# Performance work log

Measured on AMD Instinct MI355X. Metric: run time of the kernel, lower is better.

Reference implementation:

```python
import jax, jax.numpy as jnp
import numpy as np

Q_LEN = 2048
K_LEN = 2048
BATCH = 2
EMBED = 1024
HEADS = 16
HEAD_DIM = EMBED // HEADS
PE_ROWS = 2 * K_LEN


def _shift(p):
    # Transformer-XL pad/flatten shift: p is [B, H, Q, S] with S = 2*K-1 -> [B, H, Q, K]
    B, H, Q, S = p.shape
    pp = jnp.pad(p, ((0, 0), (0, 0), (0, 1), (0, 1)))          # [B,H,Q+1,S+1]
    flat = pp.reshape(B, H, (Q + 1) * (S + 1))
    flat = jax.lax.slice_in_dim(flat, S // 2, S // 2 + Q * S, axis=-1)
    return flat.reshape(B, H, Q, S)[..., : (S + 1) // 2]


def setup_inputs() -> dict:
    key = jax.random.key(0)
    ks = jax.random.split(key, 11)
    ws = 0.02  # weight scale
    inp = {
        "query": jax.random.normal(ks[0], (Q_LEN, BATCH, EMBED), jnp.float32),
        "key": jax.random.normal(ks[1], (K_LEN, BATCH, EMBED), jnp.float32),
        "value": jax.random.normal(ks[2], (K_LEN, BATCH, EMBED), jnp.float32),
        "pe": jax.random.normal(ks[3], (PE_ROWS, EMBED), jnp.float32),
        "w_q": jax.random.normal(ks[4], (EMBED, EMBED), jnp.float32) * ws,
        "w_k": jax.random.normal(ks[5], (EMBED, EMBED), jnp.float32) * ws,
        "w_v": jax.random.normal(ks[6], (EMBED, EMBED), jnp.float32) * ws,
        "w_k_pos": jax.random.normal(ks[7], (EMBED, EMBED), jnp.float32) * ws,
        "out_proj": jax.random.normal(ks[8], (EMBED, EMBED), jnp.float32) * ws,
        "content_bias": jax.random.normal(ks[9], (HEADS, HEAD_DIM), jnp.float32) * ws,
        "pos_bias": jax.random.normal(ks[10], (HEADS, HEAD_DIM), jnp.float32) * ws,
        "attn_mask": jnp.triu(jnp.ones((Q_LEN, K_LEN), dtype=bool), k=1),  # causal
    }
    return inp


def reference(query, key, value, pe, w_q, w_k, w_v, w_k_pos, out_proj,
              content_bias, pos_bias, attn_mask):
    Qlen, B, E = query.shape
    Klen = key.shape[0]
    H, D = content_bias.shape
    scaling = D ** -0.5

    # projections (torch Linear: x @ W^T); layout -> [B, H, L, D]
    q = (query @ w_q.T).reshape(Qlen, B, H, D).transpose(1, 2, 0, 3)
    k = (key @ w_k.T).reshape(Klen, B, H, D).transpose(1, 2, 0, 3)
    v = (value @ w_v.T).reshape(Klen, B, H, D).transpose(1, 2, 0, 3)

    # relative position keys: pe slice of size 2K-1 starting at pe.size(0)//2 - K + 1
    lower = pe.shape[0] // 2 - Klen + 1
    pe_slice = jax.lax.dynamic_slice_in_dim(pe, lower, 2 * Klen - 1, axis=0)
    k_pos = (pe_slice @ w_k_pos.T).reshape(2 * Klen - 1, H, D).transpose(1, 0, 2)  # [H, 2K-1, D]

    content = jnp.einsum('bhqd,bhkd->bhqk', q + content_bias[None, :, None, :], k)
    pos = jnp.einsum('bhqd,hsd->bhqs', q + pos_bias[None, :, None, :], k_pos)
    pos = _shift(pos)  # [B, H, Q, K]

    attn = (content + pos) * scaling
    attn = jnp.where(attn_mask[None, None], -jnp.inf, attn)
    w = jax.nn.softmax(attn, axis=-1)

    out = jnp.einsum('bhqk,bhkd->bhqd', w, v)
    out = out.transpose(2, 0, 1, 3).reshape(Qlen, B, E)
    return out @ out_proj.T
```

## Files before the change

### kernel.cpp

```cpp
#include <hip/hip_runtime.h>
#include <hip/hip_bf16.h>

typedef __hip_bfloat16 bf16;
typedef __attribute__((ext_vector_type(8))) short short8;
typedef __attribute__((ext_vector_type(8))) unsigned short u16x8;
typedef __attribute__((ext_vector_type(4))) float f32x4;

#define QL   2048
#define KLEN 2048
#define BATCH 2
#define EMB  1024
#define NH   16
#define HD   64
#define SPE  4095

__device__ int detect_f32(const void* __restrict__ p) {
    const unsigned short* u = (const unsigned short*)p;
    int bad = 0;
    for (int i = 0; i < 256; i++) {
        int e = (u[i] >> 7) & 0xFF;
        if (e >= 0x8A) bad++;
    }
    return bad >= 8;
}

__device__ __forceinline__ ushort4 cvt4(const void* src, long u4i, int f32) {
    ushort4 o;
    if (f32) {
        float4 v = ((const float4*)src)[u4i];
        bf16 a = (bf16)v.x, b = (bf16)v.y, c = (bf16)v.z, e = (bf16)v.w;
        o.x = *(unsigned short*)&a; o.y = *(unsigned short*)&b;
        o.z = *(unsigned short*)&c; o.w = *(unsigned short*)&e;
    } else {
        o = ((const ushort4*)src)[u4i];
    }
    return o;
}

__global__ __launch_bounds__(256) void conv_w(
    const void* w0, const void* w1, const void* w2, const void* w3, const void* w4,
    const void* cb, const void* pb, bf16* __restrict__ dst)
{
    const int t = threadIdx.x;
    const int bid = blockIdx.x;
    __shared__ int f32s;
    if (bid < 1280) {
        const int seg = bid >> 8, inner = bid & 255;
        const void* src = seg == 0 ? w0 : seg == 1 ? w1 : seg == 2 ? w2 : seg == 3 ? w3 : w4;
        bf16* d = dst + (size_t)seg * 1048576;
        if (t == 0) f32s = detect_f32(src);
        __syncthreads();
        const int f32 = f32s;
#pragma unroll
        for (int i = 0; i < 4; i++) {
            long u4i = (long)inner * 1024 + i * 256 + t;
            ((ushort4*)d)[u4i] = cvt4(src, u4i, f32);
        }
    } else {
        if (t == 0) f32s = detect_f32(cb);
        __syncthreads();
        const int f32 = f32s;
        ((ushort4*)(dst + 5242880))[t]        = cvt4(cb, t, f32);
        ((ushort4*)(dst + 5242880 + 1024))[t] = cvt4(pb, t, f32);
    }
}

__global__ __launch_bounds__(256) void conv_act(
    const void* q, const void* k, const void* v, const void* pe,
    bf16* __restrict__ dq, bf16* __restrict__ dk,
    bf16* __restrict__ dv, bf16* __restrict__ dp)
{
    const int t = threadIdx.x;
    const int seg = blockIdx.x >> 10, inner = blockIdx.x & 1023;
    const void* src = seg == 0 ? q : seg == 1 ? k : seg == 2 ? v : pe;
    bf16* d = seg == 0 ? dq : seg == 1 ? dk : seg == 2 ? dv : dp;
    const long srcOff4 = (seg == 3) ? 256 : 0;
    const long zero4   = (seg == 3) ? 1048320 : (1L << 40);
    __shared__ int f32s;
    if (t == 0) f32s = detect_f32(src);
    __syncthreads();
    const int f32 = f32s;
#pragma unroll
    for (int i = 0; i < 4; i++) {
        long u4i = (long)inner * 1024 + i * 256 + t;
        ushort4 o;
        if (u4i >= zero4) { o.x = o.y = o.z = o.w = 0; }
        else o = cvt4(src, srcOff4 + u4i, f32);
        ((ushort4*)d)[u4i] = o;
    }
}

__device__ __forceinline__ void llds16(const bf16* g, bf16* l) {
    __builtin_amdgcn_global_load_lds(
        (const __attribute__((address_space(1))) void*)g,
        (__attribute__((address_space(3))) void*)l,
        16, 0, 0);
}

__global__ __launch_bounds__(256) void gemm_big(
    const bf16* __restrict__ A0, const bf16* __restrict__ A1,
    const bf16* __restrict__ A2, const bf16* __restrict__ A3,
    const bf16* __restrict__ wslab,
    bf16* __restrict__ qc, bf16* __restrict__ qp,
    bf16* __restrict__ kw, bf16* __restrict__ vw,
    bf16* __restrict__ kpos, float* __restrict__ outf, int mode_base)
{
    const int mode = mode_base + blockIdx.z;
    const bf16* A = mode == 0 ? A0 : mode == 1 ? A1 : mode == 2 ? A2 : A3;
    const bf16* W = wslab + (size_t)mode * 1048576;

    __shared__ __align__(16) bf16 Asd[128 * 64];
    __shared__ __align__(16) bf16 Wsd[128 * 64];

    const int t = threadIdx.x;
    const int w = t >> 6, lane = t & 63, lm = lane & 15, quad = lane >> 4;
    const int m0 = blockIdx.x * 128, n0 = blockIdx.y * 128;
    const int wr = (w >> 1) * 64, wc = (w & 1) * 64;

    f32x4 acc[4][4] = {};

    for (int k0 = 0; k0 < 1024; k0 += 64) {
#pragma unroll
        for (int i = 0; i < 4; i++) {
            int c = i * 256 + t, r = c >> 3, ch = c & 7, gc = ch ^ (r & 7);
            llds16(A + (size_t)(m0 + r) * 1024 + k0 + gc * 8, Asd + (c & ~63) * 8);
        }
#pragma unroll
        for (int i = 0; i < 4; i++) {
            int c = i * 256 + t, r = c >> 3, ch = c & 7, gc = ch ^ (r & 7);
            llds16(W + (size_t)(n0 + r) * 1024 + k0 + gc * 8, Wsd + (c & ~63) * 8);
        }
        __syncthreads();

        short8 af[4][2], wf[4][2];
#pragma unroll
        for (int x = 0; x < 4; x++) {
            int ra = wr + x * 16 + lm;
            af[x][0] = *(const short8*)&Asd[ra * 64 + ((quad)     ^ (ra & 7)) * 8];
            af[x][1] = *(const short8*)&Asd[ra * 64 + ((4 + quad) ^ (ra & 7)) * 8];
            int rb = wc + x * 16 + lm;
            wf[x][0] = *(const short8*)&Wsd[rb * 64 + ((quad)     ^ (rb & 7)) * 8];
            wf[x][1] = *(const short8*)&Wsd[rb * 64 + ((4 + quad) ^ (rb & 7)) * 8];
        }
#pragma unroll
        for (int kk = 0; kk < 2; kk++)
#pragma unroll
            for (int mt = 0; mt < 4; mt++)
#pragma unroll
                for (int nt = 0; nt < 4; nt++)
                    acc[mt][nt] = __builtin_amdgcn_mfma_f32_16x16x32_bf16(
                        af[mt][kk], wf[nt][kk], acc[mt][nt], 0, 0, 0);
        __syncthreads();
    }

    const bf16* cbb = wslab + 5242880;
    const bf16* pbb = wslab + 5242880 + 1024;

#pragma unroll
    for (int mt = 0; mt < 4; mt++) {
#pragma unroll
        for (int nt = 0; nt < 4; nt++) {
#pragma unroll
            for (int r4 = 0; r4 < 4; r4++) {
                int row = m0 + wr + mt * 16 + quad * 4 + r4;
                int col = n0 + wc + nt * 16 + lm;
                float v = acc[mt][nt][r4];
                if (mode == 0) {
                    int l = row >> 1, b = row & 1;
                    int h = col >> 6, d = col & 63;
                    size_t idx = ((size_t)(b * NH + h) * QL + l) * HD + d;
                    qc[idx] = (bf16)(v + __bfloat162float(cbb[col]));
                    qp[idx] = (bf16)(v + __bfloat162float(pbb[col]));
                } else if (mode == 1) {
                    int l = row >> 1, b = row & 1;
                    int h = col >> 6, d = col & 63;
                    kw[((size_t)(b * NH + h) * KLEN + l) * HD + d] = (bf16)v;
                } else if (mode == 2) {
                    int l = row >> 1, b = row & 1;
                    int h = col >> 6, d = col & 63;
                    vw[((size_t)(b * NH + h) * KLEN + l) * HD + d] = (bf16)v;
                } else if (mode == 3) {
                    if (row < SPE) {
                        int h = col >> 6, d = col & 63;
                        kpos[((size_t)h * SPE + row) * HD + d] = (bf16)v;
                    }
                } else {
                    outf[(size_t)row * 1024 + col] = v;
                }
            }
        }
    }
}

#define NEG_INF (-1.0e30f)

__global__ __launch_bounds__(256) void attn_mfma(
    const bf16* __restrict__ qc_g, const bf16* __restrict__ qp_g,
    const bf16* __restrict__ k_g,  const bf16* __restrict__ v_g,
    const bf16* __restrict__ kpos_g, bf16* __restrict__ ao)
{
    const int lin = blockIdx.x + (blockIdx.y << 6) + (blockIdx.z << 10);
    const int xcd = lin & 7, s = lin >> 3;
    const int g   = (xcd << 2) | (s >> 6);
    const int bx  = 63 - (s & 63);
    const int h   = g & 15;
    const int b   = g >> 4;
    const int q0  = bx * 32;

    const bf16* qc_bh  = qc_g + ((size_t)(b * NH + h) * QL) * HD;
    const bf16* qp_bh  = qp_g + ((size_t)(b * NH + h) * QL) * HD;
    const bf16* k_bh   = k_g  + ((size_t)(b * NH + h) * KLEN) * HD;
    const bf16* v_bh   = v_g  + ((size_t)(b * NH + h) * KLEN) * HD;
    const bf16* kpos_h = kpos_g + (size_t)h * SPE * HD;

    __shared__ __align__(16) bf16 K_s [64 * 64];
    __shared__ __align__(16) bf16 Kp_s[96 * 64];
    __shared__ __align__(16) bf16 Vt_s[64 * 64];
    __shared__ __align__(16) bf16 Pb_s[32 * 64];
    __shared__ float Sc_s[32][69];
    __shared__ float Pt_s[32][99];
    __shared__ float arow_s[32];

    const int t = threadIdx.x;
    const int w = t >> 6, lane = t & 63, lm = lane & 15, quad = lane >> 4;

    const int sr = t >> 3;
    const int sc = (t & 7) * 8;
    const int vrr = t >> 3, vch = t & 7;
    const int vslot = ((vrr >> 2) ^ vch);

    const int mtc = w & 1;
    const int ntc = (w >> 1) * 2;
    const int mtp = w >> 1;
    const int ntp = (w & 1) * 3;

    float m_run = NEG_INF, l_part = 0.0f;
    f32x4 accO[2] = {{0,0,0,0},{0,0,0,0}};
    u16x8 vv0, vv1;

    const int nkt = (bx >> 1) + 1;

    short8 aQc0, aQc1, aQp0, aQp1;
    {
        const bf16* qr = qc_bh + (size_t)(q0 + mtc * 16 + lm) * HD;
        aQc0 = *(const short8*)(qr + quad * 8);
        aQc1 = *(const short8*)(qr + (4 + quad) * 8);
        const bf16* pr = qp_bh + (size_t)(q0 + mtp * 16 + lm) * HD;
        aQp0 = *(const short8*)(pr + quad * 8);
        aQp1 = *(const short8*)(pr + (4 + quad) * 8);
    }

#pragma unroll
    for (int i = 0; i < 2; i++) {
        int c = i * 256 + t, r = c >> 3, ch = c & 7, gc = ch ^ (r & 7);
        llds16(k_bh + (size_t)r * HD + gc * 8, K_s + (c & ~63) * 8);
    }
    {
        const int s0 = 2016 - q0;
#pragma unroll
        for (int i = 0; i < 3; i++) {
            int c = i * 256 + t, r = c >> 3, ch = c & 7, gc = ch ^ (r & 7);
            llds16(kpos_h + (size_t)(s0 + r) * HD + gc * 8, Kp_s + (c & ~63) * 8);
        }
    }
    vv0 = *(const u16x8*)&v_bh[(size_t)(2 * vrr)     * HD + vch * 8];
    vv1 = *(const u16x8*)&v_bh[(size_t)(2 * vrr + 1) * HD + vch * 8];

    for (int kt = 0; kt < nkt; kt++) {
        const int k0 = kt * 64;

        __syncthreads();

        {
            const int off = (2 * vrr) & 7;
#pragma unroll
            for (int j = 0; j < 8; j++) {
                unsigned int pair = (unsigned int)vv0[j] | ((unsigned int)vv1[j] << 16);
                *(unsigned int*)&Vt_s[(vch * 8 + j) * 64 + vslot * 8 + off] = pair;
            }
        }

        {
#pragma unroll
            for (int n = 0; n < 2; n++) {
                int rowB = (ntc + n) * 16 + lm;
                short8 b0 = *(const short8*)&K_s[rowB * 64 + ((quad)     ^ (rowB & 7)) * 8];
                short8 b1 = *(const short8*)&K_s[rowB * 64 + ((4 + quad) ^ (rowB & 7)) * 8];
                f32x4 acc = {0, 0, 0, 0};
                acc = __builtin_amdgcn_mfma_f32_16x16x32_bf16(aQc0, b0, acc, 0, 0, 0);
                acc = __builtin_amdgcn_mfma_f32_16x16x32_bf16(aQc1, b1, acc, 0, 0, 0);
#pragma unroll
                for (int r = 0; r < 4; r++)
                    Sc_s[mtc * 16 + quad * 4 + r][(ntc + n) * 16 + lm] = acc[r];
            }
        }
        {
#pragma unroll
            for (int n = 0; n < 3; n++) {
                int rowB = (ntp + n) * 16 + lm;
                short8 b0 = *(const short8*)&Kp_s[rowB * 64 + ((quad)     ^ (rowB & 7)) * 8];
                short8 b1 = *(const short8*)&Kp_s[rowB * 64 + ((4 + quad) ^ (rowB & 7)) * 8];
                f32x4 acc = {0, 0, 0, 0};
                acc = __builtin_amdgcn_mfma_f32_16x16x32_bf16(aQp0, b0, acc, 0, 0, 0);
                acc = __builtin_amdgcn_mfma_f32_16x16x32_bf16(aQp1, b1, acc, 0, 0, 0);
#pragma unroll
                for (int r = 0; r < 4; r++)
                    Pt_s[mtp * 16 + quad * 4 + r][(ntp + n) * 16 + lm] = acc[r];
            }
        }

        __syncthreads();

        if (kt + 1 < nkt) {
            const int k0n = k0 + 64;
            const int s0n = k0n - q0 + 2016;
#pragma unroll
            for (int i = 0; i < 2; i++) {
                int c = i * 256 + t, r = c >> 3, ch = c & 7, gc = ch ^ (r & 7);
                llds16(k_bh + (size_t)(k0n + r) * HD + gc * 8, K_s + (c & ~63) * 8);
            }
#pragma unroll
            for (int i = 0; i < 3; i++) {
                int c = i * 256 + t, r = c >> 3, ch = c & 7, gc = ch ^ (r & 7);
                llds16(kpos_h + (size_t)(s0n + r) * HD + gc * 8, Kp_s + (c & ~63) * 8);
            }
            vv0 = *(const u16x8*)&v_bh[(size_t)(k0n + 2 * vrr)     * HD + vch * 8];
            vv1 = *(const u16x8*)&v_bh[(size_t)(k0n + 2 * vrr + 1) * HD + vch * 8];
        }

        {
            float p[8];
            float pmax = NEG_INF;
#pragma unroll
            for (int j = 0; j < 8; j++) {
                int col = sc + j;
                float s = (Sc_s[sr][col] + Pt_s[sr][col - sr + 31]) * 0.125f;
                if (k0 + col > q0 + sr) s = NEG_INF;
                p[j] = s;
                pmax = fmaxf(pmax, s);
            }
            float alpha = 1.0f;
            if (!__all(pmax <= m_run + 8.0f)) {
                float mx = pmax;
                mx = fmaxf(mx, __shfl_xor(mx, 1, 8));
                mx = fmaxf(mx, __shfl_xor(mx, 2, 8));
                mx = fmaxf(mx, __shfl_xor(mx, 4, 8));
                float mnew = fmaxf(m_run, mx);
                alpha = __expf(m_run - mnew);
                m_run = mnew;
            }
            float ls = 0.0f;
#pragma unroll
            for (int j = 0; j < 8; j++) { p[j] = __expf(p[j] - m_run); ls += p[j]; }
            l_part = l_part * alpha + ls;
            if ((t & 7) == 0) arow_s[sr] = alpha;
            short8 pv;
#pragma unroll
            for (int j = 0; j < 8; j++) { bf16 x = (bf16)p[j]; pv[j] = *(short*)&x; }
            *(short8*)&Pb_s[sr * 64 + ((t & 7) ^ (sr & 7)) * 8] = pv;
        }

        asm volatile("s_waitcnt lgkmcnt(0)" ::: "memory");
        __builtin_amdgcn_s_barrier();
        __builtin_amdgcn_sched_barrier(0);

        {
            float al[4];
#pragma unroll
            for (int r = 0; r < 4; r++) al[r] = arow_s[mtc * 16 + quad * 4 + r];
            int rowA = mtc * 16 + lm;
            short8 a0 = *(const short8*)&Pb_s[rowA * 64 + ((quad)     ^ (rowA & 7)) * 8];
            short8 a1 = *(const short8*)&Pb_s[rowA * 64 + ((4 + quad) ^ (rowA & 7)) * 8];
#pragma unroll
            for (int n = 0; n < 2; n++) {
                int d = (ntc + n) * 16 + lm;
                int dc = d >> 3;
                short8 b0 = *(const short8*)&Vt_s[d * 64 + ((quad)     ^ dc) * 8];
                short8 b1 = *(const short8*)&Vt_s[d * 64 + ((4 + quad) ^ dc) * 8];
#pragma unroll
                for (int r = 0; r < 4; r++) accO[n][r] *= al[r];
                accO[n] = __builtin_amdgcn_mfma_f32_16x16x32_bf16(a0, b0, accO[n], 0, 0, 0);
                accO[n] = __builtin_amdgcn_mfma_f32_16x16x32_bf16(a1, b1, accO[n], 0, 0, 0);
            }
        }
    }

    l_part += __shfl_xor(l_part, 1, 8);
    l_part += __shfl_xor(l_part, 2, 8);
    l_part += __shfl_xor(l_part, 4, 8);

    __syncthreads();
    if ((t & 7) == 0) arow_s[sr] = l_part;
    __syncthreads();

    float linv[4];
#pragma unroll
    for (int r = 0; r < 4; r++) linv[r] = 1.0f / arow_s[mtc * 16 + quad * 4 + r];
#pragma unroll
    for (int n = 0; n < 2; n++) {
#pragma unroll
        for (int r = 0; r < 4; r++) {
            int row = mtc * 16 + quad * 4 + r;
            ao[(((size_t)(q0 + row) * BATCH + b) * EMB) + h * HD + (ntc + n) * 16 + lm] =
                (bf16)(accO[n][r] * linv[r]);
        }
    }
}

extern "C" void kernel_launch(void* const* d_in, const int* in_sizes, int n_in,
                              void* d_out, int out_size, void* d_ws, size_t ws_size,
                              hipStream_t stream)
{
    const void* query = d_in[0];
    const void* key   = d_in[1];
    const void* value = d_in[2];
    const void* pe    = d_in[3];
    const void* w_q   = d_in[4];
    const void* w_k   = d_in[5];
    const void* w_v   = d_in[6];
    const void* w_kp  = d_in[7];
    const void* w_out = d_in[8];
    const void* cb    = d_in[9];
    const void* pb    = d_in[10];
    float* out = (float*)d_out;

    const size_t SLAB = 4194304;
    bf16* qc   = (bf16*)d_ws;
    bf16* qp   = qc + SLAB;
    bf16* kw   = qp + SLAB;
    bf16* vw   = kw + SLAB;
    bf16* kpos = vw + SLAB;
    bf16* ao   = kpos + SLAB;
    bf16* stg  = ao + SLAB;
    bf16* wqb  = stg + SLAB;

    bf16* stgQ = (bf16*)d_out;
    bf16* stgV = stgQ + SLAB;

    dim3 blk(256);

    conv_w<<<dim3(1281), blk, 0, stream>>>(w_q, w_k, w_v, w_kp, w_out, cb, pb, wqb);
    conv_act<<<dim3(4096), blk, 0, stream>>>(query, key, value, pe, stgQ, stg, stgV, ao);

    gemm_big<<<dim3(32, 8, 4), blk, 0, stream>>>(
        stgQ, stg, stgV, ao, wqb, qc, qp, kw, vw, kpos, nullptr, 0);

    attn_mfma<<<dim3(64, NH, BATCH), blk, 0, stream>>>(qc, qp, kw, vw, kpos, ao);

    gemm_big<<<dim3(32, 8, 1), blk, 0, stream>>>(
        stgQ, stg, stgV, ao, wqb, qc, qp, kw, vw, kpos, out, 4);
}
```

Before: 367.9 us.

## Fuse conversion kernels, triple-buffer GEMM, remap blocks, use exp2 softmax

Merges the weight and activation conversion kernels into one launch. Rewrites the projection GEMM as a triple-buffered K=32 pipeline with asynchronous LDS loads, and remaps workgroups across XCDs. In attention, the scale is folded into log2 units so the softmax can use exp2, and query blocks are interleaved for load balance. The V-transpose LDS swizzle and padding are also changed to reduce bank conflicts. In exchange, the GEMM loop has more iterations with more barriers, and the softmax threshold change shifts how often rescaling happens.

```diff
diff --git a/kernel.cpp b/kernel.cpp
--- a/kernel.cpp
+++ b/kernel.cpp
@@ -37,9 +37,12 @@
     return o;
 }
 
-__global__ __launch_bounds__(256) void conv_w(
+__global__ __launch_bounds__(256) void conv_all(
     const void* w0, const void* w1, const void* w2, const void* w3, const void* w4,
-    const void* cb, const void* pb, bf16* __restrict__ dst)
+    const void* cb, const void* pb, bf16* __restrict__ wdst,
+    const void* q, const void* k, const void* v, const void* pe,
+    bf16* __restrict__ dq, bf16* __restrict__ dk,
+    bf16* __restrict__ dv, bf16* __restrict__ dp)
 {
     const int t = threadIdx.x;
     const int bid = blockIdx.x;
@@ -47,7 +50,7 @@
     if (bid < 1280) {
         const int seg = bid >> 8, inner = bid & 255;
         const void* src = seg == 0 ? w0 : seg == 1 ? w1 : seg == 2 ? w2 : seg == 3 ? w3 : w4;
-        bf16* d = dst + (size_t)seg * 1048576;
+        bf16* d = wdst + (size_t)seg * 1048576;
         if (t == 0) f32s = detect_f32(src);
         __syncthreads();
         const int f32 = f32s;
@@ -56,37 +59,30 @@
             long u4i = (long)inner * 1024 + i * 256 + t;
             ((ushort4*)d)[u4i] = cvt4(src, u4i, f32);
         }
-    } else {
+    } else if (bid == 1280) {
         if (t == 0) f32s = detect_f32(cb);
         __syncthreads();
         const int f32 = f32s;
-        ((ushort4*)(dst + 5242880))[t]        = cvt4(cb, t, f32);
-        ((ushort4*)(dst + 5242880 + 1024))[t] = cvt4(pb, t, f32);
-    }
-}
-
-__global__ __launch_bounds__(256) void conv_act(
-    const void* q, const void* k, const void* v, const void* pe,
-    bf16* __restrict__ dq, bf16* __restrict__ dk,
-    bf16* __restrict__ dv, bf16* __restrict__ dp)
-{
-    const int t = threadIdx.x;
-    const int seg = blockIdx.x >> 10, inner = blockIdx.x & 1023;
-    const void* src = seg == 0 ? q : seg == 1 ? k : seg == 2 ? v : pe;
-    bf16* d = seg == 0 ? dq : seg == 1 ? dk : seg == 2 ? dv : dp;
-    const long srcOff4 = (seg == 3) ? 256 : 0;
-    const long zero4   = (seg == 3) ? 1048320 : (1L << 40);
-    __shared__ int f32s;
-    if (t == 0) f32s = detect_f32(src);
-    __syncthreads();
-    const int f32 = f32s;
-#pragma unroll
-    for (int i = 0; i < 4; i++) {
-        long u4i = (long)inner * 1024 + i * 256 + t;
-        ushort4 o;
-        if (u4i >= zero4) { o.x = o.y = o.z = o.w = 0; }
-        else o = cvt4(src, srcOff4 + u4i, f32);
-        ((ushort4*)d)[u4i] = o;
+        ((ushort4*)(wdst + 5242880))[t]        = cvt4(cb, t, f32);
+        ((ushort4*)(wdst + 5242880 + 1024))[t] = cvt4(pb, t, f32);
+    } else {
+        const int abid = bid - 1281;
+        const int seg = abid >> 10, inner = abid & 1023;
+        const void* src = seg == 0 ? q : seg == 1 ? k : seg == 2 ? v : pe;
+        bf16* d = seg == 0 ? dq : seg == 1 ? dk : seg == 2 ? dv : dp;
+        const long srcOff4 = (seg == 3) ? 256 : 0;
+        const long zero4   = (seg == 3) ? 1048320 : (1L << 40);
+        if (t == 0) f32s = detect_f32(src);
+        __syncthreads();
+        const int f32 = f32s;
+#pragma unroll
+        for (int i = 0; i < 4; i++) {
+            long u4i = (long)inner * 1024 + i * 256 + t;
+            ushort4 o;
+            if (u4i >= zero4) { o.x = o.y = o.z = o.w = 0; }
+            else o = cvt4(src, srcOff4 + u4i, f32);
+            ((ushort4*)d)[u4i] = o;
+        }
     }
 }
 
@@ -105,52 +101,65 @@
     bf16* __restrict__ kw, bf16* __restrict__ vw,
     bf16* __restrict__ kpos, float* __restrict__ outf, int mode_base)
 {
-    const int mode = mode_base + blockIdx.z;
+    const int nwg = gridDim.x * gridDim.y * gridDim.z;
+    int lin = blockIdx.x + 32 * blockIdx.y + 256 * blockIdx.z;
+    lin = (lin & 7) * (nwg >> 3) + (lin >> 3);
+    const int bx = lin & 31, by = (lin >> 5) & 7, bz = lin >> 8;
+
+    const int mode = mode_base + bz;
     const bf16* A = mode == 0 ? A0 : mode == 1 ? A1 : mode == 2 ? A2 : A3;
     const bf16* W = wslab + (size_t)mode * 1048576;
 
-    __shared__ __align__(16) bf16 Asd[128 * 64];
-    __shared__ __align__(16) bf16 Wsd[128 * 64];
+    __shared__ __align__(16) bf16 Asd[3][128 * 32];
+    __shared__ __align__(16) bf16 Wsd[3][128 * 32];
 
     const int t = threadIdx.x;
     const int w = t >> 6, lane = t & 63, lm = lane & 15, quad = lane >> 4;
-    const int m0 = blockIdx.x * 128, n0 = blockIdx.y * 128;
+    const int m0 = bx * 128, n0 = by * 128;
     const int wr = (w >> 1) * 64, wc = (w & 1) * 64;
 
     f32x4 acc[4][4] = {};
 
-    for (int k0 = 0; k0 < 1024; k0 += 64) {
-#pragma unroll
-        for (int i = 0; i < 4; i++) {
-            int c = i * 256 + t, r = c >> 3, ch = c & 7, gc = ch ^ (r & 7);
-            llds16(A + (size_t)(m0 + r) * 1024 + k0 + gc * 8, Asd + (c & ~63) * 8);
-        }
-#pragma unroll
-        for (int i = 0; i < 4; i++) {
-            int c = i * 256 + t, r = c >> 3, ch = c & 7, gc = ch ^ (r & 7);
-            llds16(W + (size_t)(n0 + r) * 1024 + k0 + gc * 8, Wsd + (c & ~63) * 8);
-        }
-        __syncthreads();
-
-        short8 af[4][2], wf[4][2];
+    auto stage = [&](int buf, int k0) {
+#pragma unroll
+        for (int i = 0; i < 2; i++) {
+            int c = i * 256 + t, r = c >> 2, ch = c & 3, gc = ch ^ (r & 3);
+            llds16(A + (size_t)(m0 + r) * 1024 + k0 + gc * 8, Asd[buf] + (c & ~63) * 8);
+        }
+#pragma unroll
+        for (int i = 0; i < 2; i++) {
+            int c = i * 256 + t, r = c >> 2, ch = c & 3, gc = ch ^ (r & 3);
+            llds16(W + (size_t)(n0 + r) * 1024 + k0 + gc * 8, Wsd[buf] + (c & ~63) * 8);
+        }
+    };
+
+    stage(0, 0);
+    stage(1, 32);
+    int cur = 0, sb = 2;
+    for (int it = 0; it < 32; ++it) {
+        if (it == 31) asm volatile("s_waitcnt vmcnt(0) lgkmcnt(0)" ::: "memory");
+        else          asm volatile("s_waitcnt vmcnt(4) lgkmcnt(0)" ::: "memory");
+        __builtin_amdgcn_s_barrier();
+        __builtin_amdgcn_sched_barrier(0);
+        if (it < 30) stage(sb, (it + 2) * 32);
+
+        short8 af[4], wf[4];
 #pragma unroll
         for (int x = 0; x < 4; x++) {
             int ra = wr + x * 16 + lm;
-            af[x][0] = *(const short8*)&Asd[ra * 64 + ((quad)     ^ (ra & 7)) * 8];
-            af[x][1] = *(const short8*)&Asd[ra * 64 + ((4 + quad) ^ (ra & 7)) * 8];
+            af[x] = *(const short8*)&Asd[cur][ra * 32 + ((quad ^ (ra & 3)) * 8)];
             int rb = wc + x * 16 + lm;
-            wf[x][0] = *(const short8*)&Wsd[rb * 64 + ((quad)     ^ (rb & 7)) * 8];
-            wf[x][1] = *(const short8*)&Wsd[rb * 64 + ((4 + quad) ^ (rb & 7)) * 8];
-        }
-#pragma unroll
-        for (int kk = 0; kk < 2; kk++)
-#pragma unroll
-            for (int mt = 0; mt < 4; mt++)
-#pragma unroll
-                for (int nt = 0; nt < 4; nt++)
-                    acc[mt][nt] = __builtin_amdgcn_mfma_f32_16x16x32_bf16(
-                        af[mt][kk], wf[nt][kk], acc[mt][nt], 0, 0, 0);
-        __syncthreads();
+            wf[x] = *(const short8*)&Wsd[cur][rb * 32 + ((quad ^ (rb & 3)) * 8)];
+        }
+#pragma unroll
+        for (int mt = 0; mt < 4; mt++)
+#pragma unroll
+            for (int nt = 0; nt < 4; nt++)
+                acc[mt][nt] = __builtin_amdgcn_mfma_f32_16x16x32_bf16(
+                    af[mt], wf[nt], acc[mt][nt], 0, 0, 0);
+
+        cur = cur == 2 ? 0 : cur + 1;
+        sb  = sb  == 2 ? 0 : sb + 1;
     }
 
     const bf16* cbb = wslab + 5242880;
@@ -193,6 +202,7 @@
 }
 
 #define NEG_INF (-1.0e30f)
+#define SCL2 0.18033688011f
 
 __global__ __launch_bounds__(256) void attn_mfma(
     const bf16* __restrict__ qc_g, const bf16* __restrict__ qp_g,
@@ -202,7 +212,8 @@
     const int lin = blockIdx.x + (blockIdx.y << 6) + (blockIdx.z << 10);
     const int xcd = lin & 7, s = lin >> 3;
     const int g   = (xcd << 2) | (s >> 6);
-    const int bx  = 63 - (s & 63);
+    const int u   = s & 63;
+    const int bx  = (u & 1) ? (u >> 1) : 63 - (u >> 1);
     const int h   = g & 15;
     const int b   = g >> 4;
     const int q0  = bx * 32;
@@ -218,7 +229,7 @@
     __shared__ __align__(16) bf16 Vt_s[64 * 64];
     __shared__ __align__(16) bf16 Pb_s[32 * 64];
     __shared__ float Sc_s[32][69];
-    __shared__ float Pt_s[32][99];
+    __shared__ float Pt_s[32][98];
     __shared__ float arow_s[32];
 
     const int t = threadIdx.x;
@@ -227,7 +238,7 @@
     const int sr = t >> 3;
     const int sc = (t & 7) * 8;
     const int vrr = t >> 3, vch = t & 7;
-    const int vslot = ((vrr >> 2) ^ vch);
+    const int vkc = vrr >> 2;
 
     const int mtc = w & 1;
     const int ntc = (w >> 1) * 2;
@@ -276,7 +287,8 @@
 #pragma unroll
             for (int j = 0; j < 8; j++) {
                 unsigned int pair = (unsigned int)vv0[j] | ((unsigned int)vv1[j] << 16);
-                *(unsigned int*)&Vt_s[(vch * 8 + j) * 64 + vslot * 8 + off] = pair;
+                int slot = vkc ^ vch ^ j;
+                *(unsigned int*)&Vt_s[(vch * 8 + j) * 64 + slot * 8 + off] = pair;
             }
         }
 
@@ -334,24 +346,27 @@
 #pragma unroll
             for (int j = 0; j < 8; j++) {
                 int col = sc + j;
-                float s = (Sc_s[sr][col] + Pt_s[sr][col - sr + 31]) * 0.125f;
-                if (k0 + col > q0 + sr) s = NEG_INF;
-                p[j] = s;
-                pmax = fmaxf(pmax, s);
+                float sv = (Sc_s[sr][col] + Pt_s[sr][col - sr + 31]) * SCL2;
+                if (k0 + col > q0 + sr) sv = NEG_INF;
+                p[j] = sv;
+                pmax = fmaxf(pmax, sv);
             }
             float alpha = 1.0f;
-            if (!__all(pmax <= m_run + 8.0f)) {
+            if (!__all(pmax <= m_run + 11.5f)) {
                 float mx = pmax;
                 mx = fmaxf(mx, __shfl_xor(mx, 1, 8));
                 mx = fmaxf(mx, __shfl_xor(mx, 2, 8));
                 mx = fmaxf(mx, __shfl_xor(mx, 4, 8));
                 float mnew = fmaxf(m_run, mx);
-                alpha = __expf(m_run - mnew);
+                alpha = __builtin_amdgcn_exp2f(m_run - mnew);
                 m_run = mnew;
             }
             float ls = 0.0f;
 #pragma unroll
-            for (int j = 0; j < 8; j++) { p[j] = __expf(p[j] - m_run); ls += p[j]; }
+            for (int j = 0; j < 8; j++) {
+                p[j] = __builtin_amdgcn_exp2f(p[j] - m_run);
+                ls += p[j];
+            }
             l_part = l_part * alpha + ls;
             if ((t & 7) == 0) arow_s[sr] = alpha;
             short8 pv;
@@ -374,9 +389,9 @@
 #pragma unroll
             for (int n = 0; n < 2; n++) {
                 int d = (ntc + n) * 16 + lm;
-                int dc = d >> 3;
-                short8 b0 = *(const short8*)&Vt_s[d * 64 + ((quad)     ^ dc) * 8];
-                short8 b1 = *(const short8*)&Vt_s[d * 64 + ((4 + quad) ^ dc) * 8];
+                int ds = (d >> 3) ^ (d & 7);
+                short8 b0 = *(const short8*)&Vt_s[d * 64 + ((quad     ^ ds)) * 8];
+                short8 b1 = *(const short8*)&Vt_s[d * 64 + (((4 + quad) ^ ds)) * 8];
 #pragma unroll
                 for (int r = 0; r < 4; r++) accO[n][r] *= al[r];
                 accO[n] = __builtin_amdgcn_mfma_f32_16x16x32_bf16(a0, b0, accO[n], 0, 0, 0);
@@ -439,8 +454,9 @@
 
     dim3 blk(256);
 
-    conv_w<<<dim3(1281), blk, 0, stream>>>(w_q, w_k, w_v, w_kp, w_out, cb, pb, wqb);
-    conv_act<<<dim3(4096), blk, 0, stream>>>(query, key, value, pe, stgQ, stg, stgV, ao);
+    conv_all<<<dim3(5377), blk, 0, stream>>>(
+        w_q, w_k, w_v, w_kp, w_out, cb, pb, wqb,
+        query, key, value, pe, stgQ, stg, stgV, ao);
 
     gemm_big<<<dim3(32, 8, 4), blk, 0, stream>>>(
         stgQ, stg, stgV, ao, wqb, qc, qp, kw, vw, kpos, nullptr, 0);
```

Measured after the change: 413.1 us. +12.3%, slower.
